# Performance work log

Hardware: AMD Instinct MI355X
Metric: run time of the kernel (lower is better)

The kernel has to match this reference:

```python
import jax, jax.numpy as jnp
import numpy as np

N, K, C0, H = 256, 16, 16, 32  # vertices, regular degree, input feats, hidden


def setup_inputs() -> dict:
    key = jax.random.key(0)
    ks = jax.random.split(key, 4)
    # k-regular circulant graph: neighbors of i are i+/-1..i+/-K//2 (mod N), sorted by vertex id
    offs = np.concatenate([np.arange(1, K // 2 + 1), -np.arange(1, K // 2 + 1)])
    nbrs = np.sort((np.arange(N)[:, None] + offs[None, :]) % N, axis=1).astype(np.int32)
    X = jax.random.normal(ks[0], (N, C0), jnp.float32)
    W1 = jax.random.normal(ks[1], (18 * C0, H), jnp.float32) / np.sqrt(18 * C0)
    b1 = jnp.zeros((H,), jnp.float32)
    W2 = jax.random.normal(ks[2], (18 * H, H), jnp.float32) / np.sqrt(18 * H)
    b2 = jnp.zeros((H,), jnp.float32)
    fc_w = jax.random.normal(ks[3], (H, 1), jnp.float32) / np.sqrt(H)
    fc_b = jnp.zeros((1,), jnp.float32)
    return {"X": X, "nbrs": jnp.asarray(nbrs), "W1": W1, "b1": b1,
            "W2": W2, "b2": b2, "fc_w": fc_w, "fc_b": fc_b}


def contract18(T, A):
    """All 18 contractions of F6[t,a,b,e,f,c] = T[t,a,b,c] * A[e,f],
    exactly matching _collapse6to3 (_c6to2_111 + _c6to2_12 + _c6to2_3),
    without materializing the 6-d tensor.
    T: (n, k, k, k, c) with axes (vertex, t, a, b, channel); A: (k, k).
    Returns (n, k, k, 18*c)."""
    S = A.sum()            # total sum of A
    r = A.sum(1)           # row sums
    tr = jnp.trace(A)
    sum_b = T.sum(3)              # (n,t,a,c)
    sum_t = T.sum(1)              # (n,a,b,c)
    sum_ab = T.sum((2, 3))        # (n,t,c)
    sum_tb = T.sum((1, 3))        # (n,a,c)
    sum_all = T.sum((1, 2, 3))    # (n,c)
    # _c6to2_111 (5 permutations)
    c1 = sum_b * S
    c2 = sum_ab[:, :, None, :] * r[None, None, :, None]
    c3 = sum_t * S
    c4 = sum_tb[:, :, None, :] * r[None, None, :, None]
    c5 = sum_all[:, None, None, :] * A[None, :, :, None]
    # _c6to2_12 (1 nontrivial permutation + 9 identical identity permutations)
    c6 = jnp.einsum('ntabc,b->ntac', T, r)
    c7 = sum_b * tr  # repeated 9 times, as in the source
    # _c6to2_3 (3 planar-diagonal contractions)
    d_ab = jnp.diagonal(T, axis1=2, axis2=3).transpose(0, 1, 3, 2)   # (n,t,a,c): T[t,a,a,c]
    c16 = jnp.einsum('ntac,ea->ntec', d_ab, A)
    d_tb = jnp.diagonal(T, axis1=1, axis2=3)                          # (n,a,c,t): T[t,a,t,c]
    c17 = jnp.einsum('nact,et->naec', d_tb, A)
    d_ttt = jnp.einsum('ntttc->ntc', T).sum(1)                        # (n,c)
    c18 = d_ttt[:, None, None, :] * A[None, :, :, None]
    return jnp.concatenate([c1, c2, c3, c4, c5, c6] + [c7] * 9 + [c16, c17, c18], axis=-1)


def _forward(X, nbrs, W1, b1, W2, b2, fc_w, fc_b):
    n, k = nbrs.shape
    # chi_{i,t}[a,p] = 1 iff a-th neighbor of i == p-th neighbor of j, j = nbrs[i,t]
    NN = nbrs[nbrs]                                                    # (n,k,k)
    CH = (nbrs[:, None, :, None] == NN[:, :, None, :]).astype(X.dtype)  # (n,t,a,p)
    A = jnp.eye(k, dtype=X.dtype)  # chi_{i,i} is the k x k identity for every i

    # get_F0: broadcast vertex features to (n, k, k, c0)
    F = jnp.broadcast_to(X[:, None, None, :], (n, k, k, X.shape[1]))

    def layer(F, W, b):
        Fg = F[nbrs]                                             # (n,t,p,q,c) gather neighbor features
        tmp = jnp.einsum('ntap,ntpqc->ntaqc', CH, Fg)            # chi @ F
        T = jnp.einsum('ntaqc,ntbq->ntabc', tmp, CH)             # (chi @ F) @ chi^T
        col = contract18(T, A)                                   # (n,k,k,18c)
        return jax.nn.relu(col @ W + b)

    F1 = layer(F, W1, b1)
    F2 = layer(F1, W2, b2)
    # get_Troot then full sum: chi_root scatters F2 entries injectively into [n,n,c],
    # so sum over Troot == sum over all entries of F2.
    g = F2.sum((0, 1, 2))                                        # (H,)
    return g @ fc_w + fc_b                                       # (1,)


def reference(X, nbrs, W1, b1, W2, b2, fc_w, fc_b):
    return _forward(X, nbrs, W1, b1, W2, b2, fc_w, fc_b)
```

## Files before the change

### kernel.cpp

```cpp
#include <hip/hip_runtime.h>


constexpr int KN = 16, HH = 32, NV = 256, C2 = 32;

typedef float f32x2 __attribute__((ext_vector_type(2)));
typedef float f32x4 __attribute__((ext_vector_type(4)));

__device__ __forceinline__ f32x2 pkfma(f32x2 a, f32x2 b, f32x2 c) {
    f32x2 d;
    asm("v_pk_fma_f32 %0, %1, %2, %3" : "=v"(d) : "v"(a), "v"(b), "v"(c));
    return d;
}
__device__ __forceinline__ f32x2 pkfma_lo(f32x2 cf, f32x2 w, f32x2 acc) {
    f32x2 d;
    asm("v_pk_fma_f32 %0, %1, %2, %3 op_sel:[0,0,0] op_sel_hi:[0,1,1]"
        : "=v"(d) : "v"(cf), "v"(w), "v"(acc));
    return d;
}
__device__ __forceinline__ f32x2 pkfma_hi(f32x2 cf, f32x2 w, f32x2 acc) {
    f32x2 d;
    asm("v_pk_fma_f32 %0, %1, %2, %3 op_sel:[1,0,0] op_sel_hi:[1,1,1]"
        : "=v"(d) : "v"(cf), "v"(w), "v"(acc));
    return d;
}
__device__ __forceinline__ f32x2 pkadd(f32x2 a, f32x2 b) {
    f32x2 d;
    asm("v_pk_add_f32 %0, %1, %2" : "=v"(d) : "v"(a), "v"(b));
    return d;
}
__device__ __forceinline__ f32x2 pkmul(f32x2 a, f32x2 b) {
    f32x2 d;
    asm("v_pk_mul_f32 %0, %1, %2" : "=v"(d) : "v"(a), "v"(b));
    return d;
}
__device__ __forceinline__ f32x2 vlo(f32x4 v) { return __builtin_shufflevector(v, v, 0, 1); }
__device__ __forceinline__ f32x2 vhi(f32x4 v) { return __builtin_shufflevector(v, v, 2, 3); }

#define MM_DSP(WLDS, NC2, CPARR, ACC2) do {                                    \
    const f32x4* W4_ = (const f32x4*)(WLDS);                                   \
    _Pragma("unroll")                                                          \
    for (int cp = 0; cp < (NC2); ++cp) {                                       \
        const f32x2 cfp_ = (CPARR)[cp];                                        \
        _Pragma("unroll")                                                      \
        for (int h4 = 0; h4 < 8; ++h4) {                                       \
            const f32x4 w_ = W4_[(2 * cp) * 8 + h4];                           \
            (ACC2)[2*h4+0] = pkfma_lo(cfp_, vlo(w_), (ACC2)[2*h4+0]);          \
            (ACC2)[2*h4+1] = pkfma_lo(cfp_, vhi(w_), (ACC2)[2*h4+1]);          \
        }                                                                      \
        _Pragma("unroll")                                                      \
        for (int h4 = 0; h4 < 8; ++h4) {                                       \
            const f32x4 w_ = W4_[(2 * cp + 1) * 8 + h4];                       \
            (ACC2)[2*h4+0] = pkfma_hi(cfp_, vlo(w_), (ACC2)[2*h4+0]);          \
            (ACC2)[2*h4+1] = pkfma_hi(cfp_, vhi(w_), (ACC2)[2*h4+1]);          \
        }                                                                      \
    }                                                                          \
} while (0)

__global__ __launch_bounds__(512)
void ccn_l1(const float* __restrict__ X, const int* __restrict__ nbrs,
            const float* __restrict__ W1, const float* __restrict__ bias,
            float* __restrict__ F1c, float* __restrict__ outz,
            const float* __restrict__ W2f, float* __restrict__ Wsb2)
{
    __shared__ float sE1[6 * 512];
    __shared__ float sPP2[8 * 256 * 4];
    __shared__ float sX[16][20];
    __shared__ float sV[16][164];
    __shared__ float s_Z4[16][20];
    __shared__ float s_Z5[16];
    __shared__ int   s_nbi[16];
    __shared__ int   s_nbj[16][17];
    __shared__ int   s_P[16][16];
    __shared__ int   s_vm[16];
    __shared__ float s_m[16];

    const int tid  = threadIdx.x;
    const int i    = ((blockIdx.x & 7) << 5) | (blockIdx.x >> 3);

    if (blockIdx.x == 0 && tid == 0) outz[0] = 0.f;

    if (blockIdx.x < 2) {
        const int u = (blockIdx.x << 9) | tid;
        float acc = 0.f;
        #pragma unroll
        for (int g = 6; g < 15; ++g) acc += W2f[g * 1024 + u];
        Wsb2[u] = 16.f * W2f[u] + W2f[5 * 1024 + u] + 16.f * acc;
    }

    if (tid < 16) s_nbi[tid] = nbrs[i * 16 + tid];
    __syncthreads();

    if (tid < 256) {
        const int t = tid >> 4, y = tid & 15;
        const int j = s_nbi[t];
        s_nbj[t][y] = nbrs[j * 16 + y];
        sX[t][y]    = X[j * 16 + y];
    } else {
        const int u = tid - 256;
        float acc = 0.f;
        #pragma unroll
        for (int g = 6; g < 15; ++g) acc += W1[g * 512 + u];
        sE1[u]        = 16.f * W1[u] + W1[5 * 512 + u] + 16.f * acc;
        sE1[512 + u]  = W1[512 + u];
        sE1[1024 + u] = W1[15 * 512 + u];
        sE1[1536 + u] = W1[2 * 512 + u];
        sE1[2048 + u] = W1[3 * 512 + u];
        sE1[2560 + u] = W1[4 * 512 + u];
    }
    __syncthreads();

    if (tid < 256) {
        const int t = tid >> 4, y = tid & 15;
        const int tgt = s_nbi[y];
        int p = -1;
        #pragma unroll
        for (int q = 0; q < 16; ++q) if (s_nbj[t][q] == tgt) p = q;
        s_P[t][y] = p;
        unsigned long long bal = __ballot(p >= 0);
        if (y == 0) {
            int vm = (int)((bal >> ((t & 3) * 16)) & 0xFFFFull);
            s_vm[t] = vm;
            s_m[t]  = (float)__popc(vm);
        }
    } else {
        const int u = tid;
        float acc = 0.f;
        #pragma unroll
        for (int g = 6; g < 15; ++g) acc += W1[g * 512 + u];
        sE1[u]        = 16.f * W1[u] + W1[5 * 512 + u] + 16.f * acc;
        sE1[512 + u]  = W1[512 + u];
        sE1[1024 + u] = W1[15 * 512 + u];
        sE1[1536 + u] = W1[2 * 512 + u];
        sE1[2048 + u] = W1[3 * 512 + u];
        sE1[2560 + u] = W1[4 * 512 + u];
    }
    __syncthreads();

    if (tid < 256) {
        const int t = tid >> 4, c = tid & 15;
        float acc = 0.f;
        #pragma unroll
        for (int tp = 0; tp < 16; ++tp) {
            const float fb = ((s_vm[tp] >> t) & 1) ? s_m[tp] : 0.f;
            acc = fmaf(fb, sX[tp][c], acc);
        }
        s_Z4[t][c] = acc;
    } else if (tid < 272) {
        const int c = tid - 256;
        float acc = 0.f;
        #pragma unroll
        for (int tp = 0; tp < 16; ++tp) {
            const float mt = s_m[tp];
            acc = fmaf(mt * mt, sX[tp][c], acc);
        }
        s_Z5[c] = acc;
    }
    __syncthreads();

    if (tid < 256) {
        const int t = tid >> 4, y = tid & 15;
        f32x2 Y0p[8];
        #pragma unroll
        for (int c4 = 0; c4 < 4; ++c4) {
            const f32x4 v = *(const f32x4*)&sX[t][4 * c4];
            Y0p[2*c4+0] = vlo(v); Y0p[2*c4+1] = vhi(v);
        }
        const float m = s_m[t];
        const f32x2 mp2 = {m, m};
        f32x2 v0p = {0.f,0.f}, v1p = {0.f,0.f}, v2p = {0.f,0.f};
        f32x2 v3p = {0.f,0.f}, v4p = {0.f,0.f};
        const float2* Wsb = (const float2*)(sE1 + 0 * 512);
        const float2* Wab = (const float2*)(sE1 + 1 * 512);
        const float2* W16 = (const float2*)(sE1 + 2 * 512);
        const float2* Wtb = (const float2*)(sE1 + 4 * 512);
        const float2* Wal = (const float2*)(sE1 + 5 * 512);
        #pragma unroll
        for (int cp = 0; cp < 8; ++cp) {
            const f32x2 cf0p = pkmul(mp2, Y0p[cp]);
            const f32x2 cf1p = pkmul(mp2, cf0p);
            const f32x2 cf2p = Y0p[cp];
            const f32x2 cf3p = *(const f32x2*)&s_Z4[t][2 * cp];
            const f32x2 cf4p = *(const f32x2*)&s_Z5[2 * cp];
            const int i0 = (2 * cp) * 16 + y, i1 = (2 * cp + 1) * 16 + y;
            f32x2 w;
            w = *(const f32x2*)&Wsb[i0]; v0p = pkfma_lo(cf0p, w, v0p);
            w = *(const f32x2*)&Wsb[i1]; v0p = pkfma_hi(cf0p, w, v0p);
            w = *(const f32x2*)&Wab[i0]; v1p = pkfma_lo(cf1p, w, v1p);
            w = *(const f32x2*)&Wab[i1]; v1p = pkfma_hi(cf1p, w, v1p);
            w = *(const f32x2*)&W16[i0]; v2p = pkfma_lo(cf2p, w, v2p);
            w = *(const f32x2*)&W16[i1]; v2p = pkfma_hi(cf2p, w, v2p);
            w = *(const f32x2*)&Wtb[i0]; v3p = pkfma_lo(cf3p, w, v3p);
            w = *(const f32x2*)&Wtb[i1]; v3p = pkfma_hi(cf3p, w, v3p);
            w = *(const f32x2*)&Wal[i0]; v4p = pkfma_lo(cf4p, w, v4p);
            w = *(const f32x2*)&Wal[i1]; v4p = pkfma_hi(cf4p, w, v4p);
        }
        *(f32x2*)&sV[t][0 * 32 + 2 * y] = v0p;
        *(f32x2*)&sV[t][1 * 32 + 2 * y] = v1p;
        *(f32x2*)&sV[t][2 * 32 + 2 * y] = v2p;
        *(f32x2*)&sV[t][3 * 32 + 2 * y] = v3p;
        *(f32x2*)&sV[t][4 * 32 + 2 * y] = v4p;
    } else {
        const int w = tid - 256;
        const int t = w >> 4, y = w & 15, x = t;
        f32x2 Z22[8];
        #pragma unroll
        for (int c = 0; c < 8; ++c) Z22[c] = (f32x2){0.f,0.f};
        #pragma unroll
        for (int tp = 0; tp < 16; ++tp) {
            const int vm = s_vm[tp];
            const float f2 = (float)((vm >> x) & (vm >> y) & 1);
            const f32x2 f22 = {f2, f2};
            #pragma unroll
            for (int c4 = 0; c4 < 4; ++c4) {
                const f32x4 v = *(const f32x4*)&sX[tp][4 * c4];
                Z22[2*c4+0] = pkfma(f22, vlo(v), Z22[2*c4+0]);
                Z22[2*c4+1] = pkfma(f22, vhi(v), Z22[2*c4+1]);
            }
        }
        f32x2 Z22s[8];
        const f32x2 sixteen = {16.f, 16.f};
        #pragma unroll
        for (int k = 0; k < 8; ++k) Z22s[k] = pkmul(sixteen, Z22[k]);
        f32x2 pp2[16];
        #pragma unroll
        for (int h = 0; h < 16; ++h) pp2[h] = (f32x2){0.f,0.f};
        MM_DSP(sE1 + 3 * 512, 8, Z22s, pp2);
        const int cell = y * 16 + t;
        #pragma unroll
        for (int h4 = 0; h4 < 8; ++h4) {
            const int base = (h4 * 256 + cell) * 4;
            *(f32x2*)&sPP2[base]     = pp2[2*h4+0];
            *(f32x2*)&sPP2[base + 2] = pp2[2*h4+1];
        }
    }
    __syncthreads();

    if (tid < 256) {
        const int q = tid >> 4, p = tid & 15;
        const float vy  = (s_P[p][q] >= 0) ? 1.f : 0.f;
        const float dxy = (p == q) ? 1.f : 0.f;
        const f32x2 vy2 = {vy, vy}, dxy2 = {dxy, dxy};
        float4* F4 = (float4*)F1c;
        const size_t basec = ((size_t)i * 16 + q) * 128 + p;
        #pragma unroll
        for (int h4 = 0; h4 < 8; ++h4) {
            const f32x4 V0 = *(const f32x4*)&sV[p][0 * 32 + 4 * h4];
            const f32x4 V1 = *(const f32x4*)&sV[p][1 * 32 + 4 * h4];
            const f32x4 V2 = *(const f32x4*)&sV[p][2 * 32 + 4 * h4];
            const f32x4 V3 = *(const f32x4*)&sV[p][3 * 32 + 4 * h4];
            const f32x4 V4 = *(const f32x4*)&sV[p][4 * 32 + 4 * h4];
            const f32x4 PP = *(const f32x4*)&sPP2[(h4 * 256 + q * 16 + p) * 4];
            const f32x2 blo = *(const f32x2*)&bias[4 * h4];
            const f32x2 bhi = *(const f32x2*)&bias[4 * h4 + 2];
            f32x2 slo = pkadd(vlo(V0), vlo(V2));
            slo = pkfma(vy2, slo, vlo(V1));
            slo = pkadd(slo, vlo(V3));
            slo = pkfma(dxy2, vlo(V4), slo);
            slo = pkadd(slo, vlo(PP));
            slo = pkadd(slo, blo);
            f32x2 shi = pkadd(vhi(V0), vhi(V2));
            shi = pkfma(vy2, shi, vhi(V1));
            shi = pkadd(shi, vhi(V3));
            shi = pkfma(dxy2, vhi(V4), shi);
            shi = pkadd(shi, vhi(PP));
            shi = pkadd(shi, bhi);
            F4[basec + h4 * 16] = make_float4(fmaxf(slo.x, 0.f), fmaxf(slo.y, 0.f),
                                              fmaxf(shi.x, 0.f), fmaxf(shi.y, 0.f));
        }
    }
}

__global__ __launch_bounds__(512)
void ccn_l2(const float* __restrict__ F1c, const int* __restrict__ nbrs,
            const float* __restrict__ W2, const float* __restrict__ bias,
            const float* __restrict__ fcw, const float* __restrict__ fcb,
            float* __restrict__ out, const float* __restrict__ Wsb2)
{
    __shared__ float sMM[3 * 1024];
    __shared__ float sW3[3 * 1024];
    __shared__ float sRpp[256 * 34];
    __shared__ float s_stb[16 * 34];
    __shared__ float s_sab[16 * 34];
    __shared__ float s_sall[C2];
    __shared__ int   s_nbi[16];
    __shared__ int   s_PQ[16 * 17];
    __shared__ float s_red[4];

    const int tid  = threadIdx.x;
    const int i    = ((blockIdx.x & 7) << 5) | (blockIdx.x >> 3);
    const int lane = tid & 63;
    const f32x4* F4 = (const f32x4*)F1c;

    if (tid < 16) s_nbi[tid] = nbrs[i * 16 + tid];
    __syncthreads();

    if (tid < 256) {
        const int t = tid >> 4, y = tid & 15;
        const int j = s_nbi[t];
        s_PQ[t * 17 + y] = nbrs[j * 16 + y];
    } else {
        const int w = tid - 256;
        ((f32x4*)sMM)[w]       = ((const f32x4*)Wsb2)[w];
        ((f32x4*)sMM)[256 + w] = ((const f32x4*)(W2 + 15 * 1024))[w];
        ((f32x4*)sMM)[512 + w] = ((const f32x4*)(W2 +  2 * 1024))[w];
        ((f32x4*)sW3)[w]       = ((const f32x4*)(W2 +  1 * 1024))[w];
        ((f32x4*)sW3)[256 + w] = ((const f32x4*)(W2 +  3 * 1024))[w];
        ((f32x4*)sW3)[512 + w] = ((const f32x4*)(W2 +  4 * 1024))[w];
    }
    __syncthreads();

    if (tid < 256) {
        const int t = tid >> 4, y = tid & 15;
        const int tgt = s_nbi[y];
        int p = -1;
        #pragma unroll
        for (int q = 0; q < 16; ++q) if (s_PQ[t * 17 + q] == tgt) p = q;
        s_PQ[t * 17 + y] = p;
    }
    __syncthreads();

    f32x2 pre2[16];
    f32x2 pp2[16];

    if (tid < 256) {
        const int t = tid >> 4, y = tid & 15;
        const int j = s_nbi[t];
        const int p = s_PQ[t * 17 + y];
        const size_t jbase = (size_t)j * 2048;

        f32x2 R2[16];
        #pragma unroll
        for (int c = 0; c < 16; ++c) R2[c] = (f32x2){0.f, 0.f};
        if (p >= 0) {
            #pragma unroll
            for (int b = 0; b < 16; ++b) {
                const int q = s_PQ[t * 17 + b];
                if (q >= 0) {
                    const size_t rb = jbase + (size_t)q * 128 + p;
                    #pragma unroll
                    for (int c4 = 0; c4 < 8; ++c4) {
                        const f32x4 v = F4[rb + c4 * 16];
                        R2[2*c4+0] = pkadd(vlo(v), R2[2*c4+0]);
                        R2[2*c4+1] = pkadd(vhi(v), R2[2*c4+1]);
                    }
                }
            }
        }
        {
            float* dst = &sRpp[(t * 16 + y) * 34];
            #pragma unroll
            for (int c4 = 0; c4 < 8; ++c4) {
                *(f32x2*)&dst[4*c4]     = R2[2*c4+0];
                *(f32x2*)&dst[4*c4 + 2] = R2[2*c4+1];
            }
        }

        #pragma unroll
        for (int h = 0; h < 16; ++h) pre2[h] = (f32x2){0.f, 0.f};
        MM_DSP(sMM, 16, R2, pre2);

        f32x2 D2[16];
        #pragma unroll
        for (int c = 0; c < 16; ++c) D2[c] = (f32x2){0.f, 0.f};
        if (p >= 0) {
            const size_t db = jbase + (size_t)p * 128 + p;
            #pragma unroll
            for (int c4 = 0; c4 < 8; ++c4) {
                const f32x4 v = F4[db + c4 * 16];
                D2[2*c4+0] = vlo(v);
                D2[2*c4+1] = vhi(v);
            }
        }
        MM_DSP(sMM + 1024, 16, D2, pre2);
    } else {
        const int w = tid - 256;
        const int g = w >> 4, l = w & 15;
        f32x2 ST2[16];
        #pragma unroll
        for (int c = 0; c < 16; ++c) ST2[c] = (f32x2){0.f, 0.f};
        #pragma unroll
        for (int tp = 0; tp < 16; ++tp) {
            const int py = s_PQ[tp * 17 + g];
            const int px = s_PQ[tp * 17 + l];
            if (py >= 0 && px >= 0) {
                const int jt = s_nbi[tp];
                const size_t rb = (size_t)jt * 2048 + (size_t)py * 128 + px;
                #pragma unroll
                for (int c4 = 0; c4 < 8; ++c4) {
                    const f32x4 v = F4[rb + c4 * 16];
                    ST2[2*c4+0] = pkadd(vlo(v), ST2[2*c4+0]);
                    ST2[2*c4+1] = pkadd(vhi(v), ST2[2*c4+1]);
                }
            }
        }
        f32x2 ST2s[16];
        const f32x2 sixteen = {16.f, 16.f};
        #pragma unroll
        for (int k = 0; k < 16; ++k) ST2s[k] = pkmul(sixteen, ST2[k]);
        #pragma unroll
        for (int h = 0; h < 16; ++h) pp2[h] = (f32x2){0.f, 0.f};
        MM_DSP(sMM + 2048, 16, ST2s, pp2);
    }
    __syncthreads();

    if (tid < 256) {
        #pragma unroll
        for (int k = 0; k < 2; ++k) {
            const int x2 = (tid >> 5) + 8 * k;
            const int c = tid & 31;
            float s = 0.f;
            #pragma unroll
            for (int tt = 0; tt < 16; ++tt) s += sRpp[(tt * 16 + x2) * 34 + c];
            s_stb[x2 * 34 + c] = s;
        }
    } else {
        const int w = tid - 256;
        const int t = w >> 4, cp = w & 15;
        f32x2 v[16];
        #pragma unroll
        for (int yy = 0; yy < 16; ++yy)
            v[yy] = *(const f32x2*)&sRpp[(t * 16 + yy) * 34 + 2 * cp];
        f32x2 t1[8], t2[4], t3[2];
        #pragma unroll
        for (int k = 0; k < 8; ++k) t1[k] = pkadd(v[2*k], v[2*k+1]);
        #pragma unroll
        for (int k = 0; k < 4; ++k) t2[k] = pkadd(t1[2*k], t1[2*k+1]);
        #pragma unroll
        for (int k = 0; k < 2; ++k) t3[k] = pkadd(t2[2*k], t2[2*k+1]);
        *(f32x2*)&s_sab[t * 34 + 2 * cp] = pkadd(t3[0], t3[1]);
    }
    __syncthreads();

    if (tid < 256) {
        if (tid < 32) {
            float s = 0.f;
            #pragma unroll
            for (int x2 = 0; x2 < 16; ++x2) s += s_stb[x2 * 34 + tid];
            s_sall[tid] = s;
        }
    } else {
        const int w = tid - 256;
        const int g = w >> 4, l = w & 15;
        float* dst = &sRpp[(l * 16 + g) * 34];
        #pragma unroll
        for (int h4 = 0; h4 < 8; ++h4) {
            *(f32x2*)&dst[4*h4]     = pp2[2*h4+0];
            *(f32x2*)&dst[4*h4 + 2] = pp2[2*h4+1];
        }
    }
    __syncthreads();

    if (tid < 256) {
        const int t = tid >> 4, y = tid & 15, x = t;
        const float dxy = (x == y) ? 1.f : 0.f;
        f32x2 Sp = {0.f, 0.f}, Lp = {0.f, 0.f};
        {
            const float2* Wab = (const float2*)(sW3 + 0 * 1024);
            const float2* Wtb = (const float2*)(sW3 + 1 * 1024);
            const float2* Wal = (const float2*)(sW3 + 2 * 1024);
            #pragma unroll
            for (int cp = 0; cp < 16; ++cp) {
                const f32x2 cfap = *(const f32x2*)&s_sab[t * 34 + 2 * cp];
                const f32x2 cftp = *(const f32x2*)&s_stb[t * 34 + 2 * cp];
                const f32x2 cflp = *(const f32x2*)&s_sall[2 * cp];
                const int i0 = (2 * cp) * 16 + y, i1 = (2 * cp + 1) * 16 + y;
                f32x2 w;
                w = *(const f32x2*)&Wab[i0]; Sp = pkfma_lo(cfap, w, Sp);
                w = *(const f32x2*)&Wtb[i0]; Sp = pkfma_lo(cftp, w, Sp);
                w = *(const f32x2*)&Wab[i1]; Sp = pkfma_hi(cfap, w, Sp);
                w = *(const f32x2*)&Wtb[i1]; Sp = pkfma_hi(cftp, w, Sp);
                w = *(const f32x2*)&Wal[i0]; Lp = pkfma_lo(cflp, w, Lp);
                w = *(const f32x2*)&Wal[i1]; Lp = pkfma_hi(cflp, w, Lp);
            }
        }
        const float S0 = Sp.x, S1 = Sp.y, L0 = Lp.x, L1 = Lp.y;
        const int gbase = (t & 3) * 16;
        #pragma unroll
        for (int h = 0; h < HH; ++h) {
            const int src = gbase + (h >> 1);
            const float sv = (h & 1) ? S1 : S0;
            const float lv = (h & 1) ? L1 : L0;
            pre2[h >> 1][h & 1] += __shfl(sv, src, 64) + dxy * __shfl(lv, src, 64);
        }
        {
            const float* ppr = &sRpp[(t * 16 + y) * 34];
            #pragma unroll
            for (int h4 = 0; h4 < 8; ++h4) {
                const f32x2 a = *(const f32x2*)&ppr[4*h4];
                const f32x2 b = *(const f32x2*)&ppr[4*h4 + 2];
                pre2[2*h4+0] = pkadd(pre2[2*h4+0], a);
                pre2[2*h4+1] = pkadd(pre2[2*h4+1], b);
            }
        }
        float local = 0.f;
        #pragma unroll
        for (int h = 0; h < HH; ++h) {
            float v = pre2[h >> 1][h & 1] + bias[h];
            v = v > 0.f ? v : 0.f;
            local += v * fcw[h];
        }
        #pragma unroll
        for (int off = 32; off > 0; off >>= 1) local += __shfl_down(local, off, 64);
        if (lane == 0) s_red[tid >> 6] = local;
    }
    __syncthreads();
    if (tid == 0) {
        const float v = s_red[0] + s_red[1] + s_red[2] + s_red[3]
                      + fcb[0] * (1.f / 256.f);
        atomicAdd(out, v);
    }
}

extern "C" void kernel_launch(void* const* d_in, const int* in_sizes, int n_in,
                              void* d_out, int out_size, void* d_ws, size_t ws_size,
                              hipStream_t stream) {
    const float* X    = (const float*)d_in[0];
    const int*   nbrs = (const int*)  d_in[1];
    const float* W1   = (const float*)d_in[2];
    const float* b1   = (const float*)d_in[3];
    const float* W2   = (const float*)d_in[4];
    const float* b2   = (const float*)d_in[5];
    const float* fc_w = (const float*)d_in[6];
    const float* fc_b = (const float*)d_in[7];
    float* outp = (float*)d_out;

    float* F1c  = (float*)d_ws;
    float* Wsb2 = F1c + 2097152;

    ccn_l1<<<NV, 512, 0, stream>>>(X, nbrs, W1, b1, F1c, outp, W2, Wsb2);
    ccn_l2<<<NV, 512, 0, stream>>>(F1c, nbrs, W2, b2, fc_w, fc_b, outp, Wsb2);
}
```

Baseline: 104.0 us.

## Split layer-2 row gather across an extra 256-thread group

```diff
diff --git a/kernel.cpp b/kernel.cpp
--- a/kernel.cpp
+++ b/kernel.cpp
@@ -270,7 +270,7 @@
     }
 }
 
-__global__ __launch_bounds__(512)
+__global__ __launch_bounds__(768)
 void ccn_l2(const float* __restrict__ F1c, const int* __restrict__ nbrs,
             const float* __restrict__ W2, const float* __restrict__ bias,
             const float* __restrict__ fcw, const float* __restrict__ fcb,
@@ -298,11 +298,13 @@
         const int t = tid >> 4, y = tid & 15;
         const int j = s_nbi[t];
         s_PQ[t * 17 + y] = nbrs[j * 16 + y];
-    } else {
+    } else if (tid < 512) {
         const int w = tid - 256;
         ((f32x4*)sMM)[w]       = ((const f32x4*)Wsb2)[w];
         ((f32x4*)sMM)[256 + w] = ((const f32x4*)(W2 + 15 * 1024))[w];
         ((f32x4*)sMM)[512 + w] = ((const f32x4*)(W2 +  2 * 1024))[w];
+    } else {
+        const int w = tid - 512;
         ((f32x4*)sW3)[w]       = ((const f32x4*)(W2 +  1 * 1024))[w];
         ((f32x4*)sW3)[256 + w] = ((const f32x4*)(W2 +  3 * 1024))[w];
         ((f32x4*)sW3)[512 + w] = ((const f32x4*)(W2 +  4 * 1024))[w];
@@ -321,6 +323,8 @@
 
     f32x2 pre2[16];
     f32x2 pp2[16];
+    f32x2 R2h[8];
+    f32x2 ST2[16];
 
     if (tid < 256) {
         const int t = tid >> 4, y = tid & 15;
@@ -328,9 +332,8 @@
         const int p = s_PQ[t * 17 + y];
         const size_t jbase = (size_t)j * 2048;
 
-        f32x2 R2[16];
-        #pragma unroll
-        for (int c = 0; c < 16; ++c) R2[c] = (f32x2){0.f, 0.f};
+        #pragma unroll
+        for (int c = 0; c < 8; ++c) R2h[c] = (f32x2){0.f, 0.f};
         if (p >= 0) {
             #pragma unroll
             for (int b = 0; b < 16; ++b) {
@@ -338,10 +341,10 @@
                 if (q >= 0) {
                     const size_t rb = jbase + (size_t)q * 128 + p;
                     #pragma unroll
-                    for (int c4 = 0; c4 < 8; ++c4) {
+                    for (int c4 = 0; c4 < 4; ++c4) {
                         const f32x4 v = F4[rb + c4 * 16];
-                        R2[2*c4+0] = pkadd(vlo(v), R2[2*c4+0]);
-                        R2[2*c4+1] = pkadd(vhi(v), R2[2*c4+1]);
+                        R2h[2*c4+0] = pkadd(vlo(v), R2h[2*c4+0]);
+                        R2h[2*c4+1] = pkadd(vhi(v), R2h[2*c4+1]);
                     }
                 }
             }
@@ -349,33 +352,14 @@
         {
             float* dst = &sRpp[(t * 16 + y) * 34];
             #pragma unroll
-            for (int c4 = 0; c4 < 8; ++c4) {
-                *(f32x2*)&dst[4*c4]     = R2[2*c4+0];
-                *(f32x2*)&dst[4*c4 + 2] = R2[2*c4+1];
-            }
-        }
-
-        #pragma unroll
-        for (int h = 0; h < 16; ++h) pre2[h] = (f32x2){0.f, 0.f};
-        MM_DSP(sMM, 16, R2, pre2);
-
-        f32x2 D2[16];
-        #pragma unroll
-        for (int c = 0; c < 16; ++c) D2[c] = (f32x2){0.f, 0.f};
-        if (p >= 0) {
-            const size_t db = jbase + (size_t)p * 128 + p;
-            #pragma unroll
-            for (int c4 = 0; c4 < 8; ++c4) {
-                const f32x4 v = F4[db + c4 * 16];
-                D2[2*c4+0] = vlo(v);
-                D2[2*c4+1] = vhi(v);
-            }
-        }
-        MM_DSP(sMM + 1024, 16, D2, pre2);
-    } else {
+            for (int c4 = 0; c4 < 4; ++c4) {
+                *(f32x2*)&dst[4*c4]     = R2h[2*c4+0];
+                *(f32x2*)&dst[4*c4 + 2] = R2h[2*c4+1];
+            }
+        }
+    } else if (tid < 512) {
         const int w = tid - 256;
         const int g = w >> 4, l = w & 15;
-        f32x2 ST2[16];
         #pragma unroll
         for (int c = 0; c < 16; ++c) ST2[c] = (f32x2){0.f, 0.f};
         #pragma unroll
@@ -393,6 +377,75 @@
                 }
             }
         }
+    } else {
+        const int w = tid - 512;
+        const int t = w >> 4, y = w & 15;
+        const int j = s_nbi[t];
+        const int p = s_PQ[t * 17 + y];
+        const size_t jbase = (size_t)j * 2048;
+
+        f32x2 Rh[8];
+        #pragma unroll
+        for (int c = 0; c < 8; ++c) Rh[c] = (f32x2){0.f, 0.f};
+        if (p >= 0) {
+            #pragma unroll
+            for (int b = 0; b < 16; ++b) {
+                const int q = s_PQ[t * 17 + b];
+                if (q >= 0) {
+                    const size_t rb = jbase + (size_t)q * 128 + p;
+                    #pragma unroll
+                    for (int c4 = 4; c4 < 8; ++c4) {
+                        const f32x4 v = F4[rb + c4 * 16];
+                        Rh[2*(c4-4)+0] = pkadd(vlo(v), Rh[2*(c4-4)+0]);
+                        Rh[2*(c4-4)+1] = pkadd(vhi(v), Rh[2*(c4-4)+1]);
+                    }
+                }
+            }
+        }
+        {
+            float* dst = &sRpp[(t * 16 + y) * 34];
+            #pragma unroll
+            for (int c4 = 4; c4 < 8; ++c4) {
+                *(f32x2*)&dst[4*c4]     = Rh[2*(c4-4)+0];
+                *(f32x2*)&dst[4*c4 + 2] = Rh[2*(c4-4)+1];
+            }
+        }
+    }
+    __syncthreads();
+
+    if (tid < 256) {
+        const int t = tid >> 4, y = tid & 15;
+        const int j = s_nbi[t];
+        const int p = s_PQ[t * 17 + y];
+        const size_t jbase = (size_t)j * 2048;
+
+        f32x2 CF[16];
+        #pragma unroll
+        for (int k = 0; k < 8; ++k) CF[k] = R2h[k];
+        {
+            const float* row = &sRpp[(t * 16 + y) * 34];
+            #pragma unroll
+            for (int k = 8; k < 16; ++k) CF[k] = *(const f32x2*)&row[2 * k];
+        }
+
+        #pragma unroll
+        for (int h = 0; h < 16; ++h) pre2[h] = (f32x2){0.f, 0.f};
+        MM_DSP(sMM, 16, CF, pre2);
+
+        f32x2 D2[16];
+        #pragma unroll
+        for (int c = 0; c < 16; ++c) D2[c] = (f32x2){0.f, 0.f};
+        if (p >= 0) {
+            const size_t db = jbase + (size_t)p * 128 + p;
+            #pragma unroll
+            for (int c4 = 0; c4 < 8; ++c4) {
+                const f32x4 v = F4[db + c4 * 16];
+                D2[2*c4+0] = vlo(v);
+                D2[2*c4+1] = vhi(v);
+            }
+        }
+        MM_DSP(sMM + 1024, 16, D2, pre2);
+    } else if (tid < 512) {
         f32x2 ST2s[16];
         const f32x2 sixteen = {16.f, 16.f};
         #pragma unroll
@@ -413,7 +466,7 @@
             for (int tt = 0; tt < 16; ++tt) s += sRpp[(tt * 16 + x2) * 34 + c];
             s_stb[x2 * 34 + c] = s;
         }
-    } else {
+    } else if (tid < 512) {
         const int w = tid - 256;
         const int t = w >> 4, cp = w & 15;
         f32x2 v[16];
@@ -438,7 +491,7 @@
             for (int x2 = 0; x2 < 16; ++x2) s += s_stb[x2 * 34 + tid];
             s_sall[tid] = s;
         }
-    } else {
+    } else if (tid < 512) {
         const int w = tid - 256;
         const int g = w >> 4, l = w & 15;
         float* dst = &sRpp[(l * 16 + g) * 34];
@@ -528,5 +581,5 @@
     float* Wsb2 = F1c + 2097152;
 
     ccn_l1<<<NV, 512, 0, stream>>>(X, nbrs, W1, b1, F1c, outp, W2, Wsb2);
-    ccn_l2<<<NV, 512, 0, stream>>>(F1c, nbrs, W2, b2, fc_w, fc_b, outp, Wsb2);
-}
+    ccn_l2<<<NV, 768, 0, stream>>>(F1c, nbrs, W2, b2, fc_w, fc_b, outp, Wsb2);
+}
```

Measured after the change: 105.6 us. Within noise of the previous version (+1.6%).
